# Kernel tuning notes

Measured on AMD Instinct MI355X. Metric: run time of the kernel, lower is better.

## Reference

```python
import jax, jax.numpy as jnp
import numpy as np

POOL = 7        # output pooled size
SAMP = 2 * POOL # crop_and_resize sampling resolution (14)


def _bilinear_crop(feat, ys, xs):
    """feat [H,W,C]; ys,xs [N,S] sample coords in feature-map pixels -> [N,S,S,C]."""
    H, W, _ = feat.shape
    ys = jnp.clip(ys, 0.0, H - 1.0)
    xs = jnp.clip(xs, 0.0, W - 1.0)
    y0f = jnp.floor(ys); x0f = jnp.floor(xs)
    y0 = y0f.astype(jnp.int32); x0 = x0f.astype(jnp.int32)
    y1 = jnp.clip(y0 + 1, 0, H - 1); x1 = jnp.clip(x0 + 1, 0, W - 1)
    wy = (ys - y0f)[:, :, None, None]   # [N,S,1,1]
    wx = (xs - x0f)[:, None, :, None]   # [N,1,S,1]
    g = lambda yi, xi: feat[yi[:, :, None], xi[:, None, :]]  # [N,S,S,C]
    out = g(y0, x0) * (1 - wy) * (1 - wx)
    out = out + g(y0, x1) * (1 - wy) * wx
    out = out + g(y1, x0) * wy * (1 - wx)
    out = out + g(y1, x1) * wy * wx
    return out


def setup_inputs() -> dict:
    key = jax.random.key(0)
    k1, k2, k3, k4, k5 = jax.random.split(key, 5)
    Hf, Wf, C = 37, 50, 512
    N = 1000
    H_img, W_img = 600.0, 800.0
    inputs = jax.random.normal(k1, (1, Hf, Wf, C), dtype=jnp.float32)
    # random valid boxes (x1,y1,x2,y2) in image coords
    cx = jax.random.uniform(k2, (N,)) * W_img
    cy = jax.random.uniform(k3, (N,)) * H_img
    bw = jax.random.uniform(k4, (N,)) * 300.0 + 16.0
    bh = jax.random.uniform(k5, (N,)) * 300.0 + 16.0
    x1 = jnp.clip(cx - bw / 2, 0.0, W_img - 1.0)
    y1 = jnp.clip(cy - bh / 2, 0.0, H_img - 1.0)
    x2 = jnp.clip(cx + bw / 2, 0.0, W_img - 1.0)
    y2 = jnp.clip(cy + bh / 2, 0.0, H_img - 1.0)
    rois = jnp.stack([x1, y1, x2, y2], axis=1).astype(jnp.float32)
    im_size = jnp.array([600, 800], dtype=jnp.int32)  # (h, w)
    return {"inputs": inputs, "rois": rois, "im_size": im_size}


def reference(inputs, rois, im_size):
    feat = inputs[0]                       # [Hf, Wf, C]
    Hf, Wf, C = feat.shape
    h = im_size[0].astype(jnp.float32)
    w = im_size[1].astype(jnp.float32)
    # normalize boxes to [0,1] (y1, x1, y2, x2), as in roi_pool_tf
    ny1 = rois[:, 1] / h; nx1 = rois[:, 0] / w
    ny2 = rois[:, 3] / h; nx2 = rois[:, 2] / w
    # crop_and_resize sample grid (TF convention: endpoints at box corners)
    t = jnp.linspace(0.0, 1.0, SAMP, dtype=jnp.float32)          # [S]
    ys = (ny1[:, None] + (ny2 - ny1)[:, None] * t[None, :]) * (Hf - 1)  # [N,S]
    xs = (nx1[:, None] + (nx2 - nx1)[:, None] * t[None, :]) * (Wf - 1)  # [N,S]
    crops = _bilinear_crop(feat, ys, xs)   # [N,14,14,C]
    N = crops.shape[0]
    pooled = crops.reshape(N, POOL, 2, POOL, 2, C).max(axis=(2, 4))  # [N,7,7,C]
    return pooled
```

## Files before the change

### kernel.cpp

```cpp
#include <hip/hip_runtime.h>
#include <math.h>

#define HF 37
#define WF 50
#define CC 512
#define POOLD 7
#define SAMPD 14

__device__ __forceinline__ float4 lerp4(float4 a, float4 b, float t) {
    float4 r;
    r.x = a.x + t * (b.x - a.x);
    r.y = a.y + t * (b.y - a.y);
    r.z = a.z + t * (b.z - a.z);
    r.w = a.w + t * (b.w - a.w);
    return r;
}

__device__ __forceinline__ float4 max4(float4 a, float4 b) {
    float4 r;
    r.x = fmaxf(a.x, b.x);
    r.y = fmaxf(a.y, b.y);
    r.z = fmaxf(a.z, b.z);
    r.w = fmaxf(a.w, b.w);
    return r;
}

__device__ __forceinline__ void loadcol(const float* __restrict__ pbase, int col,
                                        int ro0, int ro1, int ro2, int ro3,
                                        float wya, float wyb,
                                        float4& va, float4& vb) {
    const float* p = pbase + (size_t)col * CC;
    float4 r0 = *(const float4*)(p + ro0);
    float4 r1 = *(const float4*)(p + ro1);
    float4 r2 = *(const float4*)(p + ro2);
    float4 r3 = *(const float4*)(p + ro3);
    va = lerp4(r0, r1, wya);
    vb = lerp4(r2, r3, wyb);
}

__global__ __launch_bounds__(128, 3) void roipool_kernel(
    const float* __restrict__ feat,
    const float* __restrict__ rois,
    const int*   __restrict__ im_size,
    float*       __restrict__ out,
    int N)
{
    int bid = blockIdx.x;
    int n   = bid / POOLD;
    int py  = bid - n * POOLD;
    if (n >= N) return;

    float h = (float)im_size[0];
    float w = (float)im_size[1];
    float bx1 = rois[4 * n + 0];
    float by1 = rois[4 * n + 1];
    float bx2 = rois[4 * n + 2];
    float by2 = rois[4 * n + 3];
    float ny1 = by1 / h, nx1 = bx1 / w;
    float ny2 = by2 / h, nx2 = bx2 / w;

    const float inv = 1.0f / (float)(SAMPD - 1);

    float tya = (float)(2 * py) * inv;
    float tyb = (float)(2 * py + 1) * inv;
    float ysa = (ny1 + (ny2 - ny1) * tya) * (float)(HF - 1);
    float ysb = (ny1 + (ny2 - ny1) * tyb) * (float)(HF - 1);
    ysa = fminf(fmaxf(ysa, 0.0f), (float)(HF - 1));
    ysb = fminf(fmaxf(ysb, 0.0f), (float)(HF - 1));
    float y0fa = floorf(ysa);
    float y0fb = floorf(ysb);
    float wya = ysa - y0fa;
    float wyb = ysb - y0fb;
    int iya = __builtin_amdgcn_readfirstlane((int)y0fa);
    int iyb = __builtin_amdgcn_readfirstlane((int)y0fb);
    int iya1 = min(iya + 1, HF - 1);
    int iyb1 = min(iyb + 1, HF - 1);
    int ro0 = iya  * (WF * CC);
    int ro1 = iya1 * (WF * CC);
    int ro2 = iyb  * (WF * CC);
    int ro3 = iyb1 * (WF * CC);

    const float* pbase = feat + (size_t)threadIdx.x * 4;
    float* obase = out + ((size_t)(n * POOLD + py) * POOLD) * CC + (size_t)threadIdx.x * 4;

    int pcol = -1000, ccol = -1000;
    float4 vap, vbp, vac, vbc;
    float4 m0;

    #pragma unroll
    for (int sx = 0; sx < SAMPD; ++sx) {
        float tx = (float)sx * inv;
        float xs = (nx1 + (nx2 - nx1) * tx) * (float)(WF - 1);
        xs = fminf(fmaxf(xs, 0.0f), (float)(WF - 1));
        float x0f = floorf(xs);
        float wx = xs - x0f;
        int c0 = __builtin_amdgcn_readfirstlane((int)x0f);
        int c1 = min(c0 + 1, WF - 1);

        if (c0 == ccol) {
            pcol = ccol; vap = vac; vbp = vbc;
            loadcol(pbase, c1, ro0, ro1, ro2, ro3, wya, wyb, vac, vbc);
            ccol = c1;
        } else if (c0 != pcol) {
            loadcol(pbase, c0, ro0, ro1, ro2, ro3, wya, wyb, vap, vbp);
            pcol = c0;
            loadcol(pbase, c1, ro0, ro1, ro2, ro3, wya, wyb, vac, vbc);
            ccol = c1;
        }

        float4 sa = lerp4(vap, vac, wx);
        float4 sb = lerp4(vbp, vbc, wx);
        float4 mm = max4(sa, sb);

        if (sx & 1) {
            float4 r = max4(m0, mm);
            *(float4*)(obase + (size_t)(sx >> 1) * CC) = r;
        } else {
            m0 = mm;
        }
    }
}

extern "C" void kernel_launch(void* const* d_in, const int* in_sizes, int n_in,
                              void* d_out, int out_size, void* d_ws, size_t ws_size,
                              hipStream_t stream) {
    const float* feat    = (const float*)d_in[0];
    const float* rois    = (const float*)d_in[1];
    const int*   im_size = (const int*)d_in[2];
    float* out = (float*)d_out;

    int N = in_sizes[1] / 4;
    int nblocks = N * POOLD;
    roipool_kernel<<<nblocks, 128, 0, stream>>>(feat, rois, im_size, out, N);
}
```

Before: 127.1 us.

## Deduplicate shared feature-row loads and use nontemporal output stores

The kernel checks whether the two sample rows of a pooled row share feature-map rows and picks a templated path that loads two or three rows per column instead of four. Output writes become nontemporal stores so they do not pollute the cache holding the reused feature map. The cost is three instantiations of the unrolled loop, which enlarges the code, and a uniform branch per block.

```diff
diff --git a/kernel.cpp b/kernel.cpp
--- a/kernel.cpp
+++ b/kernel.cpp
@@ -6,6 +6,8 @@
 #define CC 512
 #define POOLD 7
 #define SAMPD 14
+
+typedef float nfloat4 __attribute__((ext_vector_type(4)));
 
 __device__ __forceinline__ float4 lerp4(float4 a, float4 b, float t) {
     float4 r;
@@ -25,17 +27,83 @@
     return r;
 }
 
+__device__ __forceinline__ void store_nt4(float* p, float4 v) {
+    nfloat4 nv;
+    nv.x = v.x; nv.y = v.y; nv.z = v.z; nv.w = v.w;
+    __builtin_nontemporal_store(nv, (nfloat4*)p);
+}
+
+template <int RC>
 __device__ __forceinline__ void loadcol(const float* __restrict__ pbase, int col,
                                         int ro0, int ro1, int ro2, int ro3,
                                         float wya, float wyb,
                                         float4& va, float4& vb) {
     const float* p = pbase + (size_t)col * CC;
-    float4 r0 = *(const float4*)(p + ro0);
-    float4 r1 = *(const float4*)(p + ro1);
-    float4 r2 = *(const float4*)(p + ro2);
-    float4 r3 = *(const float4*)(p + ro3);
-    va = lerp4(r0, r1, wya);
-    vb = lerp4(r2, r3, wyb);
+    if (RC == 0) {
+        float4 rA = *(const float4*)(p + ro0);
+        float4 rB = *(const float4*)(p + ro1);
+        va = lerp4(rA, rB, wya);
+        vb = lerp4(rA, rB, wyb);
+    } else if (RC == 1) {
+        float4 rA = *(const float4*)(p + ro0);
+        float4 rB = *(const float4*)(p + ro1);
+        float4 rC = *(const float4*)(p + ro3);
+        va = lerp4(rA, rB, wya);
+        vb = lerp4(rB, rC, wyb);
+    } else {
+        float4 r0 = *(const float4*)(p + ro0);
+        float4 r1 = *(const float4*)(p + ro1);
+        float4 r2 = *(const float4*)(p + ro2);
+        float4 r3 = *(const float4*)(p + ro3);
+        va = lerp4(r0, r1, wya);
+        vb = lerp4(r2, r3, wyb);
+    }
+}
+
+template <int RC>
+__device__ __forceinline__ void run_row(const float* __restrict__ pbase,
+                                        float* __restrict__ obase,
+                                        float nx1, float nx2,
+                                        int ro0, int ro1, int ro2, int ro3,
+                                        float wya, float wyb) {
+    const float inv = 1.0f / (float)(SAMPD - 1);
+
+    int pcol = -1000, ccol = -1000;
+    float4 vap, vbp, vac, vbc;
+    float4 m0;
+
+    #pragma unroll
+    for (int sx = 0; sx < SAMPD; ++sx) {
+        float tx = (float)sx * inv;
+        float xs = (nx1 + (nx2 - nx1) * tx) * (float)(WF - 1);
+        xs = fminf(fmaxf(xs, 0.0f), (float)(WF - 1));
+        float x0f = floorf(xs);
+        float wx = xs - x0f;
+        int c0 = __builtin_amdgcn_readfirstlane((int)x0f);
+        int c1 = min(c0 + 1, WF - 1);
+
+        if (c0 == ccol) {
+            pcol = ccol; vap = vac; vbp = vbc;
+            loadcol<RC>(pbase, c1, ro0, ro1, ro2, ro3, wya, wyb, vac, vbc);
+            ccol = c1;
+        } else if (c0 != pcol) {
+            loadcol<RC>(pbase, c0, ro0, ro1, ro2, ro3, wya, wyb, vap, vbp);
+            pcol = c0;
+            loadcol<RC>(pbase, c1, ro0, ro1, ro2, ro3, wya, wyb, vac, vbc);
+            ccol = c1;
+        }
+
+        float4 sa = lerp4(vap, vac, wx);
+        float4 sb = lerp4(vbp, vbc, wx);
+        float4 mm = max4(sa, sb);
+
+        if (sx & 1) {
+            float4 r = max4(m0, mm);
+            store_nt4(obase + (size_t)(sx >> 1) * CC, r);
+        } else {
+            m0 = mm;
+        }
+    }
 }
 
 __global__ __launch_bounds__(128, 3) void roipool_kernel(
@@ -83,41 +151,12 @@
     const float* pbase = feat + (size_t)threadIdx.x * 4;
     float* obase = out + ((size_t)(n * POOLD + py) * POOLD) * CC + (size_t)threadIdx.x * 4;
 
-    int pcol = -1000, ccol = -1000;
-    float4 vap, vbp, vac, vbc;
-    float4 m0;
-
-    #pragma unroll
-    for (int sx = 0; sx < SAMPD; ++sx) {
-        float tx = (float)sx * inv;
-        float xs = (nx1 + (nx2 - nx1) * tx) * (float)(WF - 1);
-        xs = fminf(fmaxf(xs, 0.0f), (float)(WF - 1));
-        float x0f = floorf(xs);
-        float wx = xs - x0f;
-        int c0 = __builtin_amdgcn_readfirstlane((int)x0f);
-        int c1 = min(c0 + 1, WF - 1);
-
-        if (c0 == ccol) {
-            pcol = ccol; vap = vac; vbp = vbc;
-            loadcol(pbase, c1, ro0, ro1, ro2, ro3, wya, wyb, vac, vbc);
-            ccol = c1;
-        } else if (c0 != pcol) {
-            loadcol(pbase, c0, ro0, ro1, ro2, ro3, wya, wyb, vap, vbp);
-            pcol = c0;
-            loadcol(pbase, c1, ro0, ro1, ro2, ro3, wya, wyb, vac, vbc);
-            ccol = c1;
-        }
-
-        float4 sa = lerp4(vap, vac, wx);
-        float4 sb = lerp4(vbp, vbc, wx);
-        float4 mm = max4(sa, sb);
-
-        if (sx & 1) {
-            float4 r = max4(m0, mm);
-            *(float4*)(obase + (size_t)(sx >> 1) * CC) = r;
-        } else {
-            m0 = mm;
-        }
+    if (ro2 == ro0) {
+        run_row<0>(pbase, obase, nx1, nx2, ro0, ro1, ro2, ro3, wya, wyb);
+    } else if (ro2 == ro1) {
+        run_row<1>(pbase, obase, nx1, nx2, ro0, ro1, ro2, ro3, wya, wyb);
+    } else {
+        run_row<2>(pbase, obase, nx1, nx2, ro0, ro1, ro2, ro3, wya, wyb);
     }
 }
 
```

Measured after the change: 126.8 us. Within noise of the previous version (-0.2%).

## Assign one block per pooled bin with deduplicated cell loads

Applied to the files above, without the earlier changes.

Launches one block per output bin (N*49 blocks) instead of one per pooled row. Each block computes its two x and two y sample positions, classifies whether the source rows and columns coincide, and dispatches to a templated path that loads only the unique 2-4 x 2-4 cells, all issued together. Output uses nontemporal stores and launch bounds rise to 4 waves per SIMD. The aim is more parallelism and memory-level overlap, at the cost of losing column reuse across neighbouring bins and adding per-block index setup.

```diff
diff --git a/kernel.cpp b/kernel.cpp
--- a/kernel.cpp
+++ b/kernel.cpp
@@ -6,6 +6,8 @@
 #define CC 512
 #define POOLD 7
 #define SAMPD 14
+
+typedef float nfloat4 __attribute__((ext_vector_type(4)));
 
 __device__ __forceinline__ float4 lerp4(float4 a, float4 b, float t) {
     float4 r;
@@ -25,20 +27,55 @@
     return r;
 }
 
-__device__ __forceinline__ void loadcol(const float* __restrict__ pbase, int col,
-                                        int ro0, int ro1, int ro2, int ro3,
-                                        float wya, float wyb,
-                                        float4& va, float4& vb) {
-    const float* p = pbase + (size_t)col * CC;
-    float4 r0 = *(const float4*)(p + ro0);
-    float4 r1 = *(const float4*)(p + ro1);
-    float4 r2 = *(const float4*)(p + ro2);
-    float4 r3 = *(const float4*)(p + ro3);
-    va = lerp4(r0, r1, wya);
-    vb = lerp4(r2, r3, wyb);
+__device__ __forceinline__ void store_nt4(float* p, float4 v) {
+    nfloat4 nv;
+    nv.x = v.x; nv.y = v.y; nv.z = v.z; nv.w = v.w;
+    __builtin_nontemporal_store(nv, (nfloat4*)p);
 }
 
-__global__ __launch_bounds__(128, 3) void roipool_kernel(
+template <int RC, int CCASE>
+__device__ __forceinline__ void do_bin(const float* __restrict__ pbase,
+                                       float* __restrict__ optr,
+                                       int ro0, int ro1, int ro2, int ro3,
+                                       int ca0, int ca1, int cb0, int cb1,
+                                       float wya, float wyb, float wxa, float wxb)
+{
+    constexpr int NR = RC + 2;
+    constexpr int NC = CCASE + 2;
+    int rofs[NR];
+    rofs[0] = ro0; rofs[1] = ro1;
+    if constexpr (RC == 1) { rofs[2] = ro3; }
+    if constexpr (RC == 2) { rofs[2] = ro2; rofs[3] = ro3; }
+    int cofs[NC];
+    cofs[0] = ca0; cofs[1] = ca1;
+    if constexpr (CCASE == 1) { cofs[2] = cb1; }
+    if constexpr (CCASE == 2) { cofs[2] = cb0; cofs[3] = cb1; }
+
+    float4 cell[NR][NC];
+    #pragma unroll
+    for (int r = 0; r < NR; ++r) {
+        #pragma unroll
+        for (int c = 0; c < NC; ++c) {
+            cell[r][c] = *(const float4*)(pbase + rofs[r] + cofs[c]);
+        }
+    }
+
+    float4 vA[NC], vB[NC];
+    #pragma unroll
+    for (int c = 0; c < NC; ++c) {
+        vA[c] = lerp4(cell[0][c],    cell[1][c],    wya);
+        vB[c] = lerp4(cell[NR-2][c], cell[NR-1][c], wyb);
+    }
+
+    float4 s0 = lerp4(vA[0],    vA[1],    wxa);
+    float4 s1 = lerp4(vA[NC-2], vA[NC-1], wxb);
+    float4 s2 = lerp4(vB[0],    vB[1],    wxa);
+    float4 s3 = lerp4(vB[NC-2], vB[NC-1], wxb);
+
+    store_nt4(optr, max4(max4(s0, s1), max4(s2, s3)));
+}
+
+__global__ __launch_bounds__(128, 4) void roipool_kernel(
     const float* __restrict__ feat,
     const float* __restrict__ rois,
     const int*   __restrict__ im_size,
@@ -46,9 +83,11 @@
     int N)
 {
     int bid = blockIdx.x;
-    int n   = bid / POOLD;
-    int py  = bid - n * POOLD;
+    int n   = bid / (POOLD * POOLD);
     if (n >= N) return;
+    int rem = bid - n * (POOLD * POOLD);
+    int py  = rem / POOLD;
+    int px  = rem - py * POOLD;
 
     float h = (float)im_size[0];
     float w = (float)im_size[1];
@@ -61,63 +100,48 @@
 
     const float inv = 1.0f / (float)(SAMPD - 1);
 
-    float tya = (float)(2 * py) * inv;
-    float tyb = (float)(2 * py + 1) * inv;
-    float ysa = (ny1 + (ny2 - ny1) * tya) * (float)(HF - 1);
-    float ysb = (ny1 + (ny2 - ny1) * tyb) * (float)(HF - 1);
+    float ysa = (ny1 + (ny2 - ny1) * ((float)(2 * py) * inv)) * (float)(HF - 1);
+    float ysb = (ny1 + (ny2 - ny1) * ((float)(2 * py + 1) * inv)) * (float)(HF - 1);
     ysa = fminf(fmaxf(ysa, 0.0f), (float)(HF - 1));
     ysb = fminf(fmaxf(ysb, 0.0f), (float)(HF - 1));
-    float y0fa = floorf(ysa);
-    float y0fb = floorf(ysb);
-    float wya = ysa - y0fa;
-    float wyb = ysb - y0fb;
-    int iya = __builtin_amdgcn_readfirstlane((int)y0fa);
-    int iyb = __builtin_amdgcn_readfirstlane((int)y0fb);
-    int iya1 = min(iya + 1, HF - 1);
-    int iyb1 = min(iyb + 1, HF - 1);
-    int ro0 = iya  * (WF * CC);
-    int ro1 = iya1 * (WF * CC);
-    int ro2 = iyb  * (WF * CC);
-    int ro3 = iyb1 * (WF * CC);
+    float ya0 = floorf(ysa), yb0 = floorf(ysb);
+    float wya = ysa - ya0,  wyb = ysb - yb0;
+    int iya = __builtin_amdgcn_readfirstlane((int)ya0);
+    int iyb = __builtin_amdgcn_readfirstlane((int)yb0);
+    int ro0 = iya * (WF * CC);
+    int ro1 = min(iya + 1, HF - 1) * (WF * CC);
+    int ro2 = iyb * (WF * CC);
+    int ro3 = min(iyb + 1, HF - 1) * (WF * CC);
+
+    float xsa = (nx1 + (nx2 - nx1) * ((float)(2 * px) * inv)) * (float)(WF - 1);
+    float xsb = (nx1 + (nx2 - nx1) * ((float)(2 * px + 1) * inv)) * (float)(WF - 1);
+    xsa = fminf(fmaxf(xsa, 0.0f), (float)(WF - 1));
+    xsb = fminf(fmaxf(xsb, 0.0f), (float)(WF - 1));
+    float xa0 = floorf(xsa), xb0 = floorf(xsb);
+    float wxa = xsa - xa0,  wxb = xsb - xb0;
+    int ixa = __builtin_amdgcn_readfirstlane((int)xa0);
+    int ixb = __builtin_amdgcn_readfirstlane((int)xb0);
+    int ca0 = ixa * CC;
+    int ca1 = min(ixa + 1, WF - 1) * CC;
+    int cb0 = ixb * CC;
+    int cb1 = min(ixb + 1, WF - 1) * CC;
 
     const float* pbase = feat + (size_t)threadIdx.x * 4;
-    float* obase = out + ((size_t)(n * POOLD + py) * POOLD) * CC + (size_t)threadIdx.x * 4;
+    float* optr = out + (size_t)bid * CC + (size_t)threadIdx.x * 4;
 
-    int pcol = -1000, ccol = -1000;
-    float4 vap, vbp, vac, vbc;
-    float4 m0;
+    int rcase = (ro2 == ro0) ? 0 : ((ro2 == ro1) ? 1 : 2);
+    int ccase = (cb0 == ca0) ? 0 : ((cb0 == ca1) ? 1 : 2);
 
-    #pragma unroll
-    for (int sx = 0; sx < SAMPD; ++sx) {
-        float tx = (float)sx * inv;
-        float xs = (nx1 + (nx2 - nx1) * tx) * (float)(WF - 1);
-        xs = fminf(fmaxf(xs, 0.0f), (float)(WF - 1));
-        float x0f = floorf(xs);
-        float wx = xs - x0f;
-        int c0 = __builtin_amdgcn_readfirstlane((int)x0f);
-        int c1 = min(c0 + 1, WF - 1);
-
-        if (c0 == ccol) {
-            pcol = ccol; vap = vac; vbp = vbc;
-            loadcol(pbase, c1, ro0, ro1, ro2, ro3, wya, wyb, vac, vbc);
-            ccol = c1;
-        } else if (c0 != pcol) {
-            loadcol(pbase, c0, ro0, ro1, ro2, ro3, wya, wyb, vap, vbp);
-            pcol = c0;
-            loadcol(pbase, c1, ro0, ro1, ro2, ro3, wya, wyb, vac, vbc);
-            ccol = c1;
-        }
-
-        float4 sa = lerp4(vap, vac, wx);
-        float4 sb = lerp4(vbp, vbc, wx);
-        float4 mm = max4(sa, sb);
-
-        if (sx & 1) {
-            float4 r = max4(m0, mm);
-            *(float4*)(obase + (size_t)(sx >> 1) * CC) = r;
-        } else {
-            m0 = mm;
-        }
+    switch (rcase * 3 + ccase) {
+        case 0: do_bin<0,0>(pbase, optr, ro0,ro1,ro2,ro3, ca0,ca1,cb0,cb1, wya,wyb,wxa,wxb); break;
+        case 1: do_bin<0,1>(pbase, optr, ro0,ro1,ro2,ro3, ca0,ca1,cb0,cb1, wya,wyb,wxa,wxb); break;
+        case 2: do_bin<0,2>(pbase, optr, ro0,ro1,ro2,ro3, ca0,ca1,cb0,cb1, wya,wyb,wxa,wxb); break;
+        case 3: do_bin<1,0>(pbase, optr, ro0,ro1,ro2,ro3, ca0,ca1,cb0,cb1, wya,wyb,wxa,wxb); break;
+        case 4: do_bin<1,1>(pbase, optr, ro0,ro1,ro2,ro3, ca0,ca1,cb0,cb1, wya,wyb,wxa,wxb); break;
+        case 5: do_bin<1,2>(pbase, optr, ro0,ro1,ro2,ro3, ca0,ca1,cb0,cb1, wya,wyb,wxa,wxb); break;
+        case 6: do_bin<2,0>(pbase, optr, ro0,ro1,ro2,ro3, ca0,ca1,cb0,cb1, wya,wyb,wxa,wxb); break;
+        case 7: do_bin<2,1>(pbase, optr, ro0,ro1,ro2,ro3, ca0,ca1,cb0,cb1, wya,wyb,wxa,wxb); break;
+        default: do_bin<2,2>(pbase, optr, ro0,ro1,ro2,ro3, ca0,ca1,cb0,cb1, wya,wyb,wxa,wxb); break;
     }
 }
 
@@ -130,6 +154,6 @@
     float* out = (float*)d_out;
 
     int N = in_sizes[1] / 4;
-    int nblocks = N * POOLD;
+    int nblocks = N * POOLD * POOLD;
     roipool_kernel<<<nblocks, 128, 0, stream>>>(feat, rois, im_size, out, N);
 }
```

Measured after the change: 129.8 us. 1.02x slower.
